# Kernel optimization log

Hardware: AMD Instinct MI355X
Metric: run time of the kernel (lower is better)

Reference implementation:

```python
import jax, jax.numpy as jnp
import numpy as np
from functools import partial

N_NODES = 50000
BN_EPS = 1e-5


def _renumber(src, dst, mask, n_nodes):
    # Faithful to extract_batch_edge_idx: kept edges are relabeled by the rank of
    # their node id among the sorted unique node ids APPEARING in kept edges.
    m = mask.astype(jnp.int32)
    appear = jnp.zeros(n_nodes, jnp.int32)
    appear = appear.at[src].max(m)
    appear = appear.at[dst].max(m)
    new_id = jnp.cumsum(appear) - 1  # rank of each appearing node id
    s = jnp.where(mask, new_id[src], 0)
    d = jnp.where(mask, new_id[dst], 0)
    return s, d


def _gcn_conv(x, W, b, src, dst, ew, n):
    # PyG GCNConv: linear, add self-loops, symmetric normalization, scatter-add.
    xw = x @ W                                   # [n, out]
    deg = jax.ops.segment_sum(ew, dst, num_segments=n) + 1.0  # +1 self loop
    dinv = jax.lax.rsqrt(deg)
    norm = dinv[src] * dinv[dst] * ew            # masked edges -> 0 weight
    agg = jax.ops.segment_sum(norm[:, None] * xw[src], dst, num_segments=n)
    agg = agg + (dinv * dinv)[:, None] * xw      # self-loop contribution
    return agg + b


def setup_inputs() -> dict:
    key = jax.random.key(0)
    ks = jax.random.split(key, 8)
    R, N, E, B = 3, N_NODES, 1000000, 2048
    inp, hid, out = 256, 512, 256
    features = jax.random.normal(ks[0], (R, N, inp), jnp.float32)
    W1 = jax.random.normal(ks[1], (inp, hid), jnp.float32) * (1.0 / np.sqrt(inp))
    b1 = jnp.zeros((hid,), jnp.float32)
    W2 = jax.random.normal(ks[2], (hid, out), jnp.float32) * (1.0 / np.sqrt(hid))
    b2 = jnp.zeros((out,), jnp.float32)
    gamma = jnp.ones((hid,), jnp.float32)
    beta = jnp.zeros((hid,), jnp.float32)
    edge_index = jax.random.randint(ks[3], (R, 2, E), 0, N, jnp.int64)
    # distinct, sorted batch node ids (torch code iterates node values)
    batch_nodes = jnp.sort(jax.random.permutation(ks[4], N)[:B]).astype(jnp.int64)
    return {"features": features, "W1": W1, "b1": b1, "W2": W2, "b2": b2,
            "gamma": gamma, "beta": beta, "edge_index": edge_index,
            "batch_nodes": batch_nodes}


def reference(features, W1, b1, W2, b2, gamma, beta, edge_index, batch_nodes):
    R, N, _ = features.shape
    B = batch_nodes.shape[0]
    in_batch = jnp.zeros(N, bool).at[batch_nodes].set(True)
    outs = []
    for r in range(R):  # small fixed relation count
        src, dst = edge_index[r, 0], edge_index[r, 1]
        mask = in_batch[src] & in_batch[dst]
        ew = mask.astype(features.dtype)
        s, d = _renumber(src, dst, mask, N)
        x = features[r, batch_nodes]             # [B, inp]
        h = _gcn_conv(x, W1, b1, s, d, ew, B)    # [B, hid]
        # BatchNorm1d (training mode: biased batch stats)
        mu = h.mean(axis=0)
        var = h.var(axis=0)
        h = (h - mu) * jax.lax.rsqrt(var + BN_EPS) * gamma + beta
        outs.append(_gcn_conv(h, W2, b2, s, d, ew, B))  # [B, out]
    stacked = jnp.stack(outs, axis=0)            # [R, B, out]
    return stacked.reshape(B, -1)                # row-major reshape, as torch
```

## Files before the change

### kernel.cpp

```cpp
#include <hip/hip_runtime.h>
#include <hip/hip_bf16.h>
#include <stdint.h>
#include <stddef.h>

#define RNUM   3
#define NNODES 50000
#define ENUM   1000000
#define BATCH  2048
#define INP    256
#define HID    512
#define OUTC   256
#define BN_EPS 1e-5f

typedef __bf16 bf16x8 __attribute__((ext_vector_type(8)));
typedef float  f32x4  __attribute__((ext_vector_type(4)));

__device__ inline unsigned short f2bf(float f) {
    union { float f; unsigned u; } c; c.f = f;
    unsigned u = c.u;
    return (unsigned short)((u + 0x7fffu + ((u >> 16) & 1u)) >> 16);
}

__device__ inline uint4 pack8(float4 a, float4 b) {
    uint4 r;
    r.x = (unsigned)f2bf(a.x) | ((unsigned)f2bf(a.y) << 16);
    r.y = (unsigned)f2bf(a.z) | ((unsigned)f2bf(a.w) << 16);
    r.z = (unsigned)f2bf(b.x) | ((unsigned)f2bf(b.y) << 16);
    r.w = (unsigned)f2bf(b.z) | ((unsigned)f2bf(b.w) << 16);
    return r;
}

__global__ __launch_bounds__(256) void k_wt(const float* __restrict__ W1,
                                            const float* __restrict__ W2,
                                            unsigned short* __restrict__ W1T,
                                            unsigned short* __restrict__ W2T) {
    __shared__ float T[32][33];
    int z = blockIdx.z;
    const float* W = z ? W2 : W1;
    unsigned short* WT = z ? W2T : W1T;
    int K = z ? HID : INP;
    int N = z ? OUTC : HID;
    int kt = blockIdx.y, nt = blockIdx.x;
    if (kt * 32 >= K || nt * 32 >= N) return;
    int tx = threadIdx.x & 31, ty = threadIdx.x >> 5;
#pragma unroll
    for (int j = 0; j < 4; ++j)
        T[ty + j * 8][tx] = W[(size_t)(kt * 32 + ty + j * 8) * N + nt * 32 + tx];
    __syncthreads();
#pragma unroll
    for (int j = 0; j < 4; ++j)
        WT[(size_t)(nt * 32 + ty + j * 8) * K + kt * 32 + tx] = f2bf(T[tx][ty + j * 8]);
}

__global__ void k_init(int* __restrict__ inv, int* __restrict__ appear,
                       float* __restrict__ deg, float* __restrict__ musum,
                       float* __restrict__ sqsum, int* __restrict__ kcount) {
    int i = blockIdx.x * blockDim.x + threadIdx.x;
    if (i < NNODES) inv[i] = -1;
    if (i < RNUM * BATCH) { appear[i] = 0; deg[i] = 0.0f; }
    if (i < RNUM * HID)   { musum[i] = 0.0f; sqsum[i] = 0.0f; }
    if (i < RNUM)         kcount[i] = 0;
}

__global__ void k_scatter_inv(const int* __restrict__ bn, int* __restrict__ inv) {
    int i = blockIdx.x * blockDim.x + threadIdx.x;
    if (i < BATCH) inv[bn[i]] = i;
}

__global__ void k_mask(const int* __restrict__ edge_index, const int* __restrict__ inv,
                       int* __restrict__ appear, int2* __restrict__ edges,
                       int* __restrict__ kcount) {
    int z = blockIdx.z;
    const int* src = edge_index + (size_t)z * 2 * ENUM;
    const int* dst = src + ENUM;
    int2* ed = edges + (size_t)z * ENUM;
    int* app = appear + z * BATCH;
    int stride = gridDim.x * blockDim.x;
    for (int e4 = blockIdx.x * blockDim.x + threadIdx.x; e4 < ENUM / 4; e4 += stride) {
        int4 s4 = ((const int4*)src)[e4];
        int4 d4 = ((const int4*)dst)[e4];
        int ss[4] = {s4.x, s4.y, s4.z, s4.w};
        int dd[4] = {d4.x, d4.y, d4.z, d4.w};
#pragma unroll
        for (int i = 0; i < 4; ++i) {
            int ps = inv[ss[i]];
            int pd = inv[dd[i]];
            if (ps >= 0 && pd >= 0) {
                int idx = atomicAdd(kcount + z, 1);
                ed[idx] = make_int2(ps, pd);
                app[ps] = 1;
                app[pd] = 1;
            }
        }
    }
}

__global__ __launch_bounds__(1024) void k_scan2048(const int* __restrict__ appear,
                                                   int* __restrict__ rankArr) {
    __shared__ int buf[2][BATCH];
    int z = blockIdx.x;
    const int* ap = appear + z * BATCH;
    int* rk = rankArr + z * BATCH;
    int t = threadIdx.x;
    buf[0][t] = ap[t];
    buf[0][t + 1024] = ap[t + 1024];
    __syncthreads();
    int cur = 0;
    for (int off = 1; off < BATCH; off <<= 1) {
        int nxt = cur ^ 1;
        int i1 = t, i2 = t + 1024;
        buf[nxt][i1] = buf[cur][i1] + (i1 >= off ? buf[cur][i1 - off] : 0);
        buf[nxt][i2] = buf[cur][i2] + (i2 >= off ? buf[cur][i2 - off] : 0);
        __syncthreads();
        cur = nxt;
    }
    rk[t] = buf[cur][t] - 1;
    rk[t + 1024] = buf[cur][t + 1024] - 1;
}

__global__ void k_deg(int2* __restrict__ edges, const int* __restrict__ rankArr,
                      const int* __restrict__ kcount, float* __restrict__ deg) {
    int z = blockIdx.z;
    int K = kcount[z];
    int2* ed = edges + (size_t)z * ENUM;
    const int* rk = rankArr + z * BATCH;
    float* dg = deg + z * BATCH;
    int stride = gridDim.x * blockDim.x;
    for (int e = blockIdx.x * blockDim.x + threadIdx.x; e < K; e += stride) {
        int2 E = ed[e];
        int s = rk[E.x], d = rk[E.y];
        ed[e] = make_int2(s, d);
        atomicAdd(&dg[d], 1.0f);
    }
}


__global__ __launch_bounds__(256) void k_gemm1(
    const float* __restrict__ features, const int* __restrict__ bn,
    const unsigned short* __restrict__ W1T, const float* __restrict__ b1,
    const float* __restrict__ deg, float* __restrict__ xw, float* __restrict__ hbase) {
    __shared__ __align__(16) unsigned short As[64][40];
    __shared__ __align__(16) unsigned short Bs[64][40];
    int z = blockIdx.z;
    const float* feat = features + (size_t)z * NNODES * INP;
    const float* dgz = deg + z * BATCH;
    float* xwz = xw + (size_t)z * BATCH * HID;
    float* hbz = hbase + (size_t)z * BATCH * HID;
    int m0 = blockIdx.y * 64, n0 = blockIdx.x * 64;
    int t = threadIdx.x;
    int ar = t >> 2, aq = t & 3;
    int grow = bn[m0 + ar];
    const float* aptr = feat + (size_t)grow * INP + aq * 8;
    const unsigned short* bptr = W1T + (size_t)(n0 + ar) * INP + aq * 8;

    int lane = t & 63, wave = t >> 6;
    int wm = (wave & 1) * 32, wn = (wave >> 1) * 32;
    int ml = lane & 15, quad = lane >> 4, q8 = quad * 8;

    f32x4 acc[2][2] = {};
    for (int k0 = 0; k0 < INP; k0 += 32) {
        float4 a0 = *(const float4*)(aptr + k0);
        float4 a1 = *(const float4*)(aptr + k0 + 4);
        uint4 bv = *(const uint4*)(bptr + k0);
        *(uint4*)&As[ar][aq * 8] = pack8(a0, a1);
        *(uint4*)&Bs[ar][aq * 8] = bv;
        __syncthreads();
        bf16x8 af[2], bfr[2];
#pragma unroll
        for (int mi = 0; mi < 2; ++mi) af[mi]  = *(const bf16x8*)&As[wm + mi * 16 + ml][q8];
#pragma unroll
        for (int ni = 0; ni < 2; ++ni) bfr[ni] = *(const bf16x8*)&Bs[wn + ni * 16 + ml][q8];
#pragma unroll
        for (int mi = 0; mi < 2; ++mi)
#pragma unroll
            for (int ni = 0; ni < 2; ++ni)
                acc[mi][ni] = __builtin_amdgcn_mfma_f32_16x16x32_bf16(af[mi], bfr[ni], acc[mi][ni], 0, 0, 0);
        __syncthreads();
    }
#pragma unroll
    for (int mi = 0; mi < 2; ++mi)
#pragma unroll
        for (int r = 0; r < 4; ++r) {
            int row = m0 + wm + mi * 16 + quad * 4 + r;
            float d2 = 1.0f / (dgz[row] + 1.0f);
#pragma unroll
            for (int ni = 0; ni < 2; ++ni) {
                int col = n0 + wn + ni * 16 + ml;
                float c = acc[mi][ni][r];
                xwz[(size_t)row * HID + col] = c;
                hbz[(size_t)row * HID + col] = d2 * c + b1[col];
            }
        }
}

__global__ __launch_bounds__(256) void k_gemm2(
    const float* __restrict__ hbase, const float* __restrict__ rstdg,
    const float* __restrict__ shiftc, const unsigned short* __restrict__ W2T,
    const float* __restrict__ b2, const float* __restrict__ deg,
    float* __restrict__ yw, float* __restrict__ out) {
    __shared__ __align__(16) unsigned short As[64][40];
    __shared__ __align__(16) unsigned short Bs[64][40];
    int z = blockIdx.z;
    const float* hz = hbase + (size_t)z * BATCH * HID;
    const float* gz = rstdg + z * HID;
    const float* sz = shiftc + z * HID;
    const float* dgz = deg + z * BATCH;
    float* ywz = yw + (size_t)z * BATCH * OUTC;
    float* oz = out + (size_t)z * BATCH * OUTC;
    int m0 = blockIdx.y * 64, n0 = blockIdx.x * 64;
    int t = threadIdx.x;
    int ar = t >> 2, aq = t & 3;
    const float* aptr = hz + (size_t)(m0 + ar) * HID + aq * 8;
    const unsigned short* bptr = W2T + (size_t)(n0 + ar) * HID + aq * 8;

    int lane = t & 63, wave = t >> 6;
    int wm = (wave & 1) * 32, wn = (wave >> 1) * 32;
    int ml = lane & 15, quad = lane >> 4, q8 = quad * 8;

    f32x4 acc[2][2] = {};
    for (int k0 = 0; k0 < HID; k0 += 32) {
        float4 h0 = *(const float4*)(aptr + k0);
        float4 h1 = *(const float4*)(aptr + k0 + 4);
        float4 g0 = *(const float4*)(gz + k0 + aq * 8);
        float4 g1 = *(const float4*)(gz + k0 + aq * 8 + 4);
        float4 s0 = *(const float4*)(sz + k0 + aq * 8);
        float4 s1 = *(const float4*)(sz + k0 + aq * 8 + 4);
        float4 a0 = make_float4(h0.x * g0.x + s0.x, h0.y * g0.y + s0.y,
                                h0.z * g0.z + s0.z, h0.w * g0.w + s0.w);
        float4 a1 = make_float4(h1.x * g1.x + s1.x, h1.y * g1.y + s1.y,
                                h1.z * g1.z + s1.z, h1.w * g1.w + s1.w);
        uint4 bv = *(const uint4*)(bptr + k0);
        *(uint4*)&As[ar][aq * 8] = pack8(a0, a1);
        *(uint4*)&Bs[ar][aq * 8] = bv;
        __syncthreads();
        bf16x8 af[2], bfr[2];
#pragma unroll
        for (int mi = 0; mi < 2; ++mi) af[mi]  = *(const bf16x8*)&As[wm + mi * 16 + ml][q8];
#pragma unroll
        for (int ni = 0; ni < 2; ++ni) bfr[ni] = *(const bf16x8*)&Bs[wn + ni * 16 + ml][q8];
#pragma unroll
        for (int mi = 0; mi < 2; ++mi)
#pragma unroll
            for (int ni = 0; ni < 2; ++ni)
                acc[mi][ni] = __builtin_amdgcn_mfma_f32_16x16x32_bf16(af[mi], bfr[ni], acc[mi][ni], 0, 0, 0);
        __syncthreads();
    }
#pragma unroll
    for (int mi = 0; mi < 2; ++mi)
#pragma unroll
        for (int r = 0; r < 4; ++r) {
            int row = m0 + wm + mi * 16 + quad * 4 + r;
            float d2 = 1.0f / (dgz[row] + 1.0f);
#pragma unroll
            for (int ni = 0; ni < 2; ++ni) {
                int col = n0 + wn + ni * 16 + ml;
                float c = acc[mi][ni][r];
                ywz[(size_t)row * OUTC + col] = c;
                oz[(size_t)row * OUTC + col] = d2 * c + b2[col];
            }
        }
}

__global__ void k_agg(const int2* __restrict__ edges, const int* __restrict__ kcount,
                      const float* __restrict__ deg, const float* __restrict__ src_mat,
                      float* __restrict__ dst_mat, int ncol) {
    int z = blockIdx.z;
    int K = kcount[z];
    const int2* ed = edges + (size_t)z * ENUM;
    const float* dgz = deg + z * BATCH;
    const float* sm = src_mat + (size_t)z * BATCH * ncol;
    float* dm = dst_mat + (size_t)z * BATCH * ncol;
    for (int e = blockIdx.x; e < K; e += gridDim.x) {
        int2 E = ed[e];
        float w = rsqrtf(dgz[E.x] + 1.0f) * rsqrtf(dgz[E.y] + 1.0f);
        const float* srow = sm + (size_t)E.x * ncol;
        float* drow = dm + (size_t)E.y * ncol;
        for (int c = threadIdx.x; c < ncol; c += blockDim.x)
            atomicAdd(&drow[c], w * srow[c]);
    }
}

__global__ __launch_bounds__(256) void k_bnstats(const float* __restrict__ hbase,
                                                 float* __restrict__ musum,
                                                 float* __restrict__ sqsum) {
    int z = blockIdx.z;
    const float* h = hbase + (size_t)z * BATCH * HID;
    int c0 = threadIdx.x;
    int r0 = blockIdx.x * 32;
    float s1a = 0, s2a = 0, s1b = 0, s2b = 0;
    for (int rr = 0; rr < 32; ++rr) {
        const float* row = h + (size_t)(r0 + rr) * HID;
        float va = row[c0];
        float vb = row[c0 + 256];
        s1a += va; s2a += va * va;
        s1b += vb; s2b += vb * vb;
    }
    atomicAdd(&musum[z * HID + c0], s1a);       atomicAdd(&sqsum[z * HID + c0], s2a);
    atomicAdd(&musum[z * HID + c0 + 256], s1b); atomicAdd(&sqsum[z * HID + c0 + 256], s2b);
}

__global__ void k_bnfinal(const float* __restrict__ musum, const float* __restrict__ sqsum,
                          const float* __restrict__ gamma, const float* __restrict__ beta,
                          float* __restrict__ rstdg, float* __restrict__ shiftc) {
    int z = blockIdx.x;
    int c = threadIdx.x;
    float mu = musum[z * HID + c] * (1.0f / BATCH);
    float ex2 = sqsum[z * HID + c] * (1.0f / BATCH);
    float var = ex2 - mu * mu;
    float g = rsqrtf(var + BN_EPS) * gamma[c];
    rstdg[z * HID + c] = g;
    shiftc[z * HID + c] = beta[c] - mu * g;
}

extern "C" void kernel_launch(void* const* d_in, const int* in_sizes, int n_in,
                              void* d_out, int out_size, void* d_ws, size_t ws_size,
                              hipStream_t stream) {
    const float* features    = (const float*)d_in[0];
    const float* W1          = (const float*)d_in[1];
    const float* b1          = (const float*)d_in[2];
    const float* W2          = (const float*)d_in[3];
    const float* b2          = (const float*)d_in[4];
    const float* gamma       = (const float*)d_in[5];
    const float* beta        = (const float*)d_in[6];
    const int*   edge_index  = (const int*)d_in[7];
    const int*   batch_nodes = (const int*)d_in[8];
    float* out = (float*)d_out;

    char* p = (char*)d_ws;
    size_t cur = 0;
    auto alloc = [&](size_t bytes) {
        void* r = p + cur;
        cur = (cur + bytes + 255) & ~(size_t)255;
        return r;
    };
    int*   inv    = (int*)  alloc(NNODES * sizeof(int));
    int*   appear = (int*)  alloc(RNUM * BATCH * sizeof(int));
    int*   rankA  = (int*)  alloc(RNUM * BATCH * sizeof(int));
    int*   kcount = (int*)  alloc(RNUM * sizeof(int));
    float* deg    = (float*)alloc(RNUM * BATCH * sizeof(float));
    float* musum  = (float*)alloc(RNUM * HID * sizeof(float));
    float* sqsum  = (float*)alloc(RNUM * HID * sizeof(float));
    float* rstdg  = (float*)alloc(RNUM * HID * sizeof(float));
    float* shiftc = (float*)alloc(RNUM * HID * sizeof(float));
    unsigned short* W1T = (unsigned short*)alloc((size_t)HID * INP * sizeof(unsigned short));
    unsigned short* W2T = (unsigned short*)alloc((size_t)OUTC * HID * sizeof(unsigned short));
    int2*  edges  = (int2*) alloc((size_t)RNUM * ENUM * sizeof(int2));
    float* xw     = (float*)alloc((size_t)RNUM * BATCH * HID * sizeof(float));
    float* hbase  = (float*)alloc((size_t)RNUM * BATCH * HID * sizeof(float));
    float* yw     = (float*)alloc((size_t)RNUM * BATCH * OUTC * sizeof(float));
    (void)ws_size; (void)in_sizes; (void)n_in; (void)out_size;

    k_wt<<<dim3(16, 16, 2), 256, 0, stream>>>(W1, W2, W1T, W2T);
    k_init<<<(NNODES + 255) / 256, 256, 0, stream>>>(inv, appear, deg, musum, sqsum, kcount);
    k_scatter_inv<<<BATCH / 256, 256, 0, stream>>>(batch_nodes, inv);

    k_mask<<<dim3(512, 1, RNUM), 256, 0, stream>>>(edge_index, inv, appear, edges, kcount);
    k_scan2048<<<RNUM, 1024, 0, stream>>>(appear, rankA);
    k_deg<<<dim3(64, 1, RNUM), 256, 0, stream>>>(edges, rankA, kcount, deg);

    k_gemm1<<<dim3(HID / 64, BATCH / 64, RNUM), 256, 0, stream>>>(
        features, batch_nodes, W1T, b1, deg, xw, hbase);
    k_agg<<<dim3(256, 1, RNUM), 256, 0, stream>>>(edges, kcount, deg, xw, hbase, HID);

    k_bnstats<<<dim3(64, 1, RNUM), 256, 0, stream>>>(hbase, musum, sqsum);
    k_bnfinal<<<RNUM, HID, 0, stream>>>(musum, sqsum, gamma, beta, rstdg, shiftc);

    k_gemm2<<<dim3(OUTC / 64, BATCH / 64, RNUM), 256, 0, stream>>>(
        hbase, rstdg, shiftc, W2T, b2, deg, yw, out);
    k_agg<<<dim3(256, 1, RNUM), 256, 0, stream>>>(edges, kcount, deg, yw, out, OUTC);
}
```

Measured before the change: 328.1 us.

## Fuse whole GCN pipeline into one cooperative persistent kernel with grid syncs

Replaces about a dozen separate kernel launches with a single cooperative kernel of 768 blocks. The phases are separated by grid.sync: weight transpose and feature bf16 conversion, bitmap-based edge masking, rank/degree computation, GEMM1, aggregation, BN stats, GEMM2 with BN folded in, and a final aggregation. The goal is to remove launch overhead and inter-kernel gaps, and to cut random lookups by using an LDS bitmap for batch membership. The cost is that serial phases leave most blocks idle, degree counting now runs on only 3 blocks, and aggregation changes to one edge per block. The old multi-kernel path is kept as a fallback if the cooperative launch fails.

```diff
diff --git a/kernel.cpp b/kernel.cpp
--- a/kernel.cpp
+++ b/kernel.cpp
@@ -1,7 +1,10 @@
 #include <hip/hip_runtime.h>
+#include <hip/hip_cooperative_groups.h>
 #include <hip/hip_bf16.h>
 #include <stdint.h>
 #include <stddef.h>
+
+namespace cg = cooperative_groups;
 
 #define RNUM   3
 #define NNODES 50000
@@ -11,6 +14,9 @@
 #define HID    512
 #define OUTC   256
 #define BN_EPS 1e-5f
+#define NBLK   768
+#define NTHR   256
+#define BMW    1568
 
 typedef __bf16 bf16x8 __attribute__((ext_vector_type(8)));
 typedef float  f32x4  __attribute__((ext_vector_type(4)));
@@ -29,6 +35,316 @@
     r.w = (unsigned)f2bf(b.z) | ((unsigned)f2bf(b.w) << 16);
     return r;
 }
+
+__global__ __launch_bounds__(NTHR, 3) void k_mega(
+    const float* __restrict__ features, const float* __restrict__ W1,
+    const float* __restrict__ b1, const float* __restrict__ W2,
+    const float* __restrict__ b2, const float* __restrict__ gamma,
+    const float* __restrict__ beta, const int* __restrict__ edge_index,
+    const int* __restrict__ bn,
+    int* inv, int* appear, int* kcount, float* deg,
+    float* musum, float* sqsum, unsigned* bitmap,
+    unsigned short* W1T, unsigned short* W2T, unsigned short* featB,
+    int2* edges, float* xw, float* hbase, float* yw, float* out) {
+
+    cg::grid_group grid = cg::this_grid();
+    __shared__ __align__(16) unsigned char smem[16896];
+    __shared__ int wsums[4];
+    const int tid = threadIdx.x;
+    const int bid = blockIdx.x;
+
+    if (bid == 0) {
+        for (int i = tid; i < BMW; i += NTHR) bitmap[i] = 0u;
+        __syncthreads();
+        for (int i = tid; i < BATCH; i += NTHR) {
+            int v = bn[i];
+            atomicOr(&bitmap[v >> 5], 1u << (v & 31));
+        }
+    } else if (bid == 1) {
+        for (int i = tid; i < BATCH; i += NTHR) inv[bn[i]] = i;
+        for (int i = tid; i < RNUM * BATCH; i += NTHR) appear[i] = 0;
+        for (int i = tid; i < RNUM * HID; i += NTHR) { musum[i] = 0.f; sqsum[i] = 0.f; }
+        if (tid < RNUM) kcount[tid] = 0;
+    }
+    if (bid < 256) {
+        float* T = (float*)smem;
+        int i = bid;
+        int z = i >> 7; i &= 127;
+        const float* W = z ? W2 : W1;
+        unsigned short* WT = z ? W2T : W1T;
+        int K = z ? HID : INP;
+        int N = z ? OUTC : HID;
+        int kt, nt;
+        if (z == 0) { nt = i & 15; kt = i >> 4; } else { nt = i & 7; kt = i >> 3; }
+        int tx = tid & 31, ty = tid >> 5;
+#pragma unroll
+        for (int j = 0; j < 4; ++j)
+            T[(ty + j * 8) * 33 + tx] = W[(size_t)(kt * 32 + ty + j * 8) * N + nt * 32 + tx];
+        __syncthreads();
+#pragma unroll
+        for (int j = 0; j < 4; ++j)
+            WT[(size_t)(nt * 32 + ty + j * 8) * K + kt * 32 + tx] = f2bf(T[tx * 33 + ty + j * 8]);
+    } else if (bid < 640) {
+        int i = bid - 256;
+        int row = i * 16 + (tid >> 4);
+        int c0 = (tid & 15) * 16;
+        int z = row >> 11, m = row & 2047;
+        const float* srow = features + ((size_t)z * NNODES + bn[m]) * INP;
+        unsigned short* drow = featB + (size_t)row * INP;
+        float4 f0 = *(const float4*)(srow + c0);
+        float4 f1 = *(const float4*)(srow + c0 + 4);
+        float4 f2 = *(const float4*)(srow + c0 + 8);
+        float4 f3 = *(const float4*)(srow + c0 + 12);
+        *(uint4*)(drow + c0)     = pack8(f0, f1);
+        *(uint4*)(drow + c0 + 8) = pack8(f2, f3);
+    }
+    grid.sync();
+
+    {
+        unsigned* bmL = (unsigned*)smem;
+        for (int i = tid; i < BMW; i += NTHR) bmL[i] = bitmap[i];
+        __syncthreads();
+        const int gsz = NBLK * NTHR;
+        const int g0 = bid * NTHR + tid;
+        for (int z = 0; z < RNUM; ++z) {
+            const int4* s4 = (const int4*)(edge_index + (size_t)z * 2 * ENUM);
+            const int4* d4 = (const int4*)(edge_index + (size_t)z * 2 * ENUM + ENUM);
+            int2* ed = edges + (size_t)z * ENUM;
+            int* app = appear + z * BATCH;
+            for (int i = g0; i < ENUM / 4; i += gsz) {
+                int4 S = s4[i], D = d4[i];
+                int ss[4] = {S.x, S.y, S.z, S.w};
+                int dd[4] = {D.x, D.y, D.z, D.w};
+#pragma unroll
+                for (int u = 0; u < 4; ++u) {
+                    int s = ss[u], d = dd[u];
+                    unsigned ks = (bmL[s >> 5] >> (s & 31)) & 1u;
+                    unsigned kd = (bmL[d >> 5] >> (d & 31)) & 1u;
+                    if (ks & kd) {
+                        int ps = inv[s], pd = inv[d];
+                        int idx = atomicAdd(&kcount[z], 1);
+                        ed[idx] = make_int2(ps, pd);
+                        app[ps] = 1;
+                        app[pd] = 1;
+                    }
+                }
+            }
+        }
+    }
+    grid.sync();
+
+    if (bid < RNUM) {
+        int z = bid;
+        int* rk    = (int*)smem;
+        float* dgf = (float*)(smem + 8192);
+        const int* ap = appear + z * BATCH;
+        int b0 = tid * 8;
+        int pre[8]; int run = 0;
+#pragma unroll
+        for (int j = 0; j < 8; ++j) { run += ap[b0 + j]; pre[j] = run; }
+        int lane = tid & 63, wv = tid >> 6;
+        int sc = run;
+        for (int off = 1; off < 64; off <<= 1) {
+            int n = __shfl_up(sc, off);
+            if (lane >= off) sc += n;
+        }
+        if (lane == 63) wsums[wv] = sc;
+        __syncthreads();
+        int base = sc - run;
+        for (int w = 0; w < wv; ++w) base += wsums[w];
+#pragma unroll
+        for (int j = 0; j < 8; ++j) { rk[b0 + j] = base + pre[j] - 1; dgf[b0 + j] = 0.f; }
+        __syncthreads();
+        int K = kcount[z];
+        int2* ed = edges + (size_t)z * ENUM;
+        for (int e = tid; e < K; e += NTHR) {
+            int2 E = ed[e];
+            int s = rk[E.x], d = rk[E.y];
+            ed[e] = make_int2(s, d);
+            atomicAdd(&dgf[d], 1.0f);
+        }
+        __syncthreads();
+        float* dz = deg + z * BATCH;
+        for (int i = tid; i < BATCH; i += NTHR) dz[i] = dgf[i];
+    }
+    grid.sync();
+
+    {
+        __syncthreads();
+        unsigned short* As = (unsigned short*)smem;
+        unsigned short* Bs = (unsigned short*)(smem + 5120);
+        int z = bid >> 8;
+        int r = bid & 255;
+        int n0 = (r & 7) * 64, m0 = (r >> 3) * 64;
+        int ar = tid >> 2, aq = tid & 3;
+        const unsigned short* aptr = featB + (size_t)(z * BATCH + m0 + ar) * INP + aq * 8;
+        const unsigned short* bptr = W1T + (size_t)(n0 + ar) * INP + aq * 8;
+        int lane = tid & 63, wave = tid >> 6;
+        int wm = (wave & 1) * 32, wn = (wave >> 1) * 32;
+        int ml = lane & 15, quad = lane >> 4, q8 = quad * 8;
+        f32x4 acc[2][2] = {};
+        for (int k0 = 0; k0 < INP; k0 += 32) {
+            uint4 av = *(const uint4*)(aptr + k0);
+            uint4 bv = *(const uint4*)(bptr + k0);
+            *(uint4*)&As[ar * 40 + aq * 8] = av;
+            *(uint4*)&Bs[ar * 40 + aq * 8] = bv;
+            __syncthreads();
+            bf16x8 af[2], bfr[2];
+#pragma unroll
+            for (int mi = 0; mi < 2; ++mi) af[mi]  = *(const bf16x8*)&As[(wm + mi * 16 + ml) * 40 + q8];
+#pragma unroll
+            for (int ni = 0; ni < 2; ++ni) bfr[ni] = *(const bf16x8*)&Bs[(wn + ni * 16 + ml) * 40 + q8];
+#pragma unroll
+            for (int mi = 0; mi < 2; ++mi)
+#pragma unroll
+                for (int ni = 0; ni < 2; ++ni)
+                    acc[mi][ni] = __builtin_amdgcn_mfma_f32_16x16x32_bf16(af[mi], bfr[ni], acc[mi][ni], 0, 0, 0);
+            __syncthreads();
+        }
+        const float* dgz = deg + z * BATCH;
+        float* xwz = xw + (size_t)z * BATCH * HID;
+        float* hbz = hbase + (size_t)z * BATCH * HID;
+#pragma unroll
+        for (int mi = 0; mi < 2; ++mi)
+#pragma unroll
+            for (int rr = 0; rr < 4; ++rr) {
+                int row = m0 + wm + mi * 16 + quad * 4 + rr;
+                float d2 = 1.0f / (dgz[row] + 1.0f);
+#pragma unroll
+                for (int ni = 0; ni < 2; ++ni) {
+                    int col = n0 + wn + ni * 16 + ml;
+                    float c = acc[mi][ni][rr];
+                    xwz[(size_t)row * HID + col] = c;
+                    hbz[(size_t)row * HID + col] = d2 * c + b1[col];
+                }
+            }
+    }
+    grid.sync();
+
+    for (int z = 0; z < RNUM; ++z) {
+        int K = kcount[z];
+        const int2* ed = edges + (size_t)z * ENUM;
+        const float* dgz = deg + z * BATCH;
+        const float* sm_ = xw + (size_t)z * BATCH * HID;
+        float* dm = hbase + (size_t)z * BATCH * HID;
+        for (int e = bid; e < K; e += NBLK) {
+            int2 E = ed[e];
+            float w = rsqrtf(dgz[E.x] + 1.0f) * rsqrtf(dgz[E.y] + 1.0f);
+            const float* srow = sm_ + (size_t)E.x * HID;
+            float* drow = dm + (size_t)E.y * HID;
+            for (int c = tid; c < HID; c += NTHR)
+                atomicAdd(&drow[c], w * srow[c]);
+        }
+    }
+    grid.sync();
+
+    if (bid < RNUM * 64) {
+        int z = bid >> 6;
+        int chunk = bid & 63;
+        const float* h = hbase + (size_t)z * BATCH * HID;
+        int c0 = tid;
+        int r0 = chunk * 32;
+        float s1a = 0, s2a = 0, s1b = 0, s2b = 0;
+        for (int rr = 0; rr < 32; ++rr) {
+            const float* row = h + (size_t)(r0 + rr) * HID;
+            float va = row[c0];
+            float vb = row[c0 + 256];
+            s1a += va; s2a += va * va;
+            s1b += vb; s2b += vb * vb;
+        }
+        atomicAdd(&musum[z * HID + c0], s1a);       atomicAdd(&sqsum[z * HID + c0], s2a);
+        atomicAdd(&musum[z * HID + c0 + 256], s1b); atomicAdd(&sqsum[z * HID + c0 + 256], s2b);
+    }
+    grid.sync();
+
+    if (bid < 384) {
+        unsigned short* As = (unsigned short*)smem;
+        unsigned short* Bs = (unsigned short*)(smem + 5120);
+        float* gL = (float*)(smem + 10240);
+        float* sL = (float*)(smem + 12288);
+        int z = bid >> 7;
+        int r = bid & 127;
+        int n0 = (r & 3) * 64, m0 = (r >> 2) * 64;
+        for (int c = tid; c < HID; c += NTHR) {
+            float mu  = musum[z * HID + c] * (1.0f / BATCH);
+            float ex2 = sqsum[z * HID + c] * (1.0f / BATCH);
+            float var = ex2 - mu * mu;
+            float g = rsqrtf(var + BN_EPS) * gamma[c];
+            gL[c] = g;
+            sL[c] = beta[c] - mu * g;
+        }
+        __syncthreads();
+        int ar = tid >> 2, aq = tid & 3;
+        const float* aptr = hbase + (size_t)z * BATCH * HID + (size_t)(m0 + ar) * HID + aq * 8;
+        const unsigned short* bptr = W2T + (size_t)(n0 + ar) * HID + aq * 8;
+        int lane = tid & 63, wave = tid >> 6;
+        int wm = (wave & 1) * 32, wn = (wave >> 1) * 32;
+        int ml = lane & 15, quad = lane >> 4, q8 = quad * 8;
+        f32x4 acc[2][2] = {};
+        for (int k0 = 0; k0 < HID; k0 += 32) {
+            float4 h0 = *(const float4*)(aptr + k0);
+            float4 h1 = *(const float4*)(aptr + k0 + 4);
+            float4 g0 = *(const float4*)(gL + k0 + aq * 8);
+            float4 g1 = *(const float4*)(gL + k0 + aq * 8 + 4);
+            float4 s0 = *(const float4*)(sL + k0 + aq * 8);
+            float4 s1 = *(const float4*)(sL + k0 + aq * 8 + 4);
+            float4 a0 = make_float4(h0.x * g0.x + s0.x, h0.y * g0.y + s0.y,
+                                    h0.z * g0.z + s0.z, h0.w * g0.w + s0.w);
+            float4 a1 = make_float4(h1.x * g1.x + s1.x, h1.y * g1.y + s1.y,
+                                    h1.z * g1.z + s1.z, h1.w * g1.w + s1.w);
+            uint4 bv = *(const uint4*)(bptr + k0);
+            *(uint4*)&As[ar * 40 + aq * 8] = pack8(a0, a1);
+            *(uint4*)&Bs[ar * 40 + aq * 8] = bv;
+            __syncthreads();
+            bf16x8 af[2], bfr[2];
+#pragma unroll
+            for (int mi = 0; mi < 2; ++mi) af[mi]  = *(const bf16x8*)&As[(wm + mi * 16 + ml) * 40 + q8];
+#pragma unroll
+            for (int ni = 0; ni < 2; ++ni) bfr[ni] = *(const bf16x8*)&Bs[(wn + ni * 16 + ml) * 40 + q8];
+#pragma unroll
+            for (int mi = 0; mi < 2; ++mi)
+#pragma unroll
+                for (int ni = 0; ni < 2; ++ni)
+                    acc[mi][ni] = __builtin_amdgcn_mfma_f32_16x16x32_bf16(af[mi], bfr[ni], acc[mi][ni], 0, 0, 0);
+            __syncthreads();
+        }
+        const float* dgz = deg + z * BATCH;
+        float* ywz = yw + (size_t)z * BATCH * OUTC;
+        float* oz = out + (size_t)z * BATCH * OUTC;
+#pragma unroll
+        for (int mi = 0; mi < 2; ++mi)
+#pragma unroll
+            for (int rr = 0; rr < 4; ++rr) {
+                int row = m0 + wm + mi * 16 + quad * 4 + rr;
+                float d2 = 1.0f / (dgz[row] + 1.0f);
+#pragma unroll
+                for (int ni = 0; ni < 2; ++ni) {
+                    int col = n0 + wn + ni * 16 + ml;
+                    float c = acc[mi][ni][rr];
+                    ywz[(size_t)row * OUTC + col] = c;
+                    oz[(size_t)row * OUTC + col] = d2 * c + b2[col];
+                }
+            }
+    }
+    grid.sync();
+
+    for (int z = 0; z < RNUM; ++z) {
+        int K = kcount[z];
+        const int2* ed = edges + (size_t)z * ENUM;
+        const float* dgz = deg + z * BATCH;
+        const float* sm_ = yw + (size_t)z * BATCH * OUTC;
+        float* dm = out + (size_t)z * BATCH * OUTC;
+        for (int e = bid; e < K; e += NBLK) {
+            int2 E = ed[e];
+            float w = rsqrtf(dgz[E.x] + 1.0f) * rsqrtf(dgz[E.y] + 1.0f);
+            const float* srow = sm_ + (size_t)E.x * OUTC;
+            float* drow = dm + (size_t)E.y * OUTC;
+            for (int c = tid; c < OUTC; c += NTHR)
+                atomicAdd(&drow[c], w * srow[c]);
+        }
+    }
+}
+
 
 __global__ __launch_bounds__(256) void k_wt(const float* __restrict__ W1,
                                             const float* __restrict__ W2,
@@ -133,7 +449,6 @@
         atomicAdd(&dg[d], 1.0f);
     }
 }
-
 
 __global__ __launch_bounds__(256) void k_gemm1(
     const float* __restrict__ features, const int* __restrict__ bn,
@@ -342,30 +657,44 @@
     float* sqsum  = (float*)alloc(RNUM * HID * sizeof(float));
     float* rstdg  = (float*)alloc(RNUM * HID * sizeof(float));
     float* shiftc = (float*)alloc(RNUM * HID * sizeof(float));
+    unsigned* bitmap = (unsigned*)alloc(BMW * sizeof(unsigned));
     unsigned short* W1T = (unsigned short*)alloc((size_t)HID * INP * sizeof(unsigned short));
     unsigned short* W2T = (unsigned short*)alloc((size_t)OUTC * HID * sizeof(unsigned short));
+    unsigned short* featB = (unsigned short*)alloc((size_t)RNUM * BATCH * INP * sizeof(unsigned short));
     int2*  edges  = (int2*) alloc((size_t)RNUM * ENUM * sizeof(int2));
     float* xw     = (float*)alloc((size_t)RNUM * BATCH * HID * sizeof(float));
     float* hbase  = (float*)alloc((size_t)RNUM * BATCH * HID * sizeof(float));
     float* yw     = (float*)alloc((size_t)RNUM * BATCH * OUTC * sizeof(float));
     (void)ws_size; (void)in_sizes; (void)n_in; (void)out_size;
 
-    k_wt<<<dim3(16, 16, 2), 256, 0, stream>>>(W1, W2, W1T, W2T);
-    k_init<<<(NNODES + 255) / 256, 256, 0, stream>>>(inv, appear, deg, musum, sqsum, kcount);
-    k_scatter_inv<<<BATCH / 256, 256, 0, stream>>>(batch_nodes, inv);
-
-    k_mask<<<dim3(512, 1, RNUM), 256, 0, stream>>>(edge_index, inv, appear, edges, kcount);
-    k_scan2048<<<RNUM, 1024, 0, stream>>>(appear, rankA);
-    k_deg<<<dim3(64, 1, RNUM), 256, 0, stream>>>(edges, rankA, kcount, deg);
-
-    k_gemm1<<<dim3(HID / 64, BATCH / 64, RNUM), 256, 0, stream>>>(
-        features, batch_nodes, W1T, b1, deg, xw, hbase);
-    k_agg<<<dim3(256, 1, RNUM), 256, 0, stream>>>(edges, kcount, deg, xw, hbase, HID);
-
-    k_bnstats<<<dim3(64, 1, RNUM), 256, 0, stream>>>(hbase, musum, sqsum);
-    k_bnfinal<<<RNUM, HID, 0, stream>>>(musum, sqsum, gamma, beta, rstdg, shiftc);
-
-    k_gemm2<<<dim3(OUTC / 64, BATCH / 64, RNUM), 256, 0, stream>>>(
-        hbase, rstdg, shiftc, W2T, b2, deg, yw, out);
-    k_agg<<<dim3(256, 1, RNUM), 256, 0, stream>>>(edges, kcount, deg, yw, out, OUTC);
-}
+    void* kargs[] = {
+        (void*)&features, (void*)&W1, (void*)&b1, (void*)&W2, (void*)&b2,
+        (void*)&gamma, (void*)&beta, (void*)&edge_index, (void*)&batch_nodes,
+        (void*)&inv, (void*)&appear, (void*)&kcount, (void*)&deg,
+        (void*)&musum, (void*)&sqsum, (void*)&bitmap,
+        (void*)&W1T, (void*)&W2T, (void*)&featB,
+        (void*)&edges, (void*)&xw, (void*)&hbase, (void*)&yw, (void*)&out};
+
+    hipError_t err = hipLaunchCooperativeKernel((const void*)k_mega, dim3(NBLK),
+                                                dim3(NTHR), kargs, 0, stream);
+    if (err != hipSuccess) {
+        k_wt<<<dim3(16, 16, 2), 256, 0, stream>>>(W1, W2, W1T, W2T);
+        k_init<<<(NNODES + 255) / 256, 256, 0, stream>>>(inv, appear, deg, musum, sqsum, kcount);
+        k_scatter_inv<<<BATCH / 256, 256, 0, stream>>>(batch_nodes, inv);
+
+        k_mask<<<dim3(512, 1, RNUM), 256, 0, stream>>>(edge_index, inv, appear, edges, kcount);
+        k_scan2048<<<RNUM, 1024, 0, stream>>>(appear, rankA);
+        k_deg<<<dim3(64, 1, RNUM), 256, 0, stream>>>(edges, rankA, kcount, deg);
+
+        k_gemm1<<<dim3(HID / 64, BATCH / 64, RNUM), 256, 0, stream>>>(
+            features, batch_nodes, W1T, b1, deg, xw, hbase);
+        k_agg<<<dim3(256, 1, RNUM), 256, 0, stream>>>(edges, kcount, deg, xw, hbase, HID);
+
+        k_bnstats<<<dim3(64, 1, RNUM), 256, 0, stream>>>(hbase, musum, sqsum);
+        k_bnfinal<<<RNUM, HID, 0, stream>>>(musum, sqsum, gamma, beta, rstdg, shiftc);
+
+        k_gemm2<<<dim3(OUTC / 64, BATCH / 64, RNUM), 256, 0, stream>>>(
+            hbase, rstdg, shiftc, W2T, b2, deg, yw, out);
+        k_agg<<<dim3(256, 1, RNUM), 256, 0, stream>>>(edges, kcount, deg, yw, out, OUTC);
+    }
+}
```

After: 920.8 us. 181% more time.
